# Performance work log

Hardware: AMD Instinct MI355X
Metric: run time of the kernel (lower is better)

## Reference

```python
import jax, jax.numpy as jnp
import numpy as np

N = 100000      # nodes
E = 1600000     # edges (avg degree 16)
IN = 128        # in_channels
H = 4           # heads
C = 32          # out_channels per head
NEG_SLOPE = 0.2 # PyG GATConv default


def setup_inputs() -> dict:
    key = jax.random.key(0)
    k = jax.random.split(key, 6)
    x = jax.random.normal(k[0], (N, IN), jnp.float32)
    edge_index = jax.random.randint(k[1], (2, E), 0, N, jnp.int32)
    # Learned params of GATConv: linear weight, per-head attention vectors, bias
    W = jax.random.normal(k[2], (IN, H * C), jnp.float32) / np.sqrt(IN)
    a_src = jax.random.normal(k[3], (H, C), jnp.float32) * 0.1
    a_dst = jax.random.normal(k[4], (H, C), jnp.float32) * 0.1
    bias = jnp.zeros((H * C,), jnp.float32)
    return {"x": x, "edge_index": edge_index, "W": W,
            "a_src": a_src, "a_dst": a_dst, "bias": bias}


def reference(x, edge_index, W, a_src, a_dst, bias):
    n = x.shape[0]
    # Linear transform, per-head view: [N, H, C]
    h = (x @ W).reshape(n, H, C)
    # Node-level attention halves: alpha_i = <h_i, a>  -> [N, H]
    alpha_src = jnp.einsum('nhc,hc->nh', h, a_src)
    alpha_dst = jnp.einsum('nhc,hc->nh', h, a_dst)
    # add_self_loops=True (PyG default)
    loops = jnp.arange(n, dtype=edge_index.dtype)
    src = jnp.concatenate([edge_index[0], loops])  # [E+N]
    dst = jnp.concatenate([edge_index[1], loops])
    # Edge attention logits with LeakyReLU: [E+N, H]
    e = jax.nn.leaky_relu(alpha_src[src] + alpha_dst[dst], NEG_SLOPE)
    # Numerically stable softmax over incoming edges of each destination node
    m = jax.ops.segment_max(e, dst, num_segments=n)          # [N, H]
    e = jnp.exp(e - m[dst])
    denom = jax.ops.segment_sum(e, dst, num_segments=n)      # [N, H]
    att = e / denom[dst]                                     # [E+N, H]
    # Weighted scatter-aggregate of source features: [N, H, C]
    out = jax.ops.segment_sum(att[:, :, None] * h[src], dst, num_segments=n)
    # concat=True: flatten heads, add bias
    return out.reshape(n, H * C) + bias
```

## Files before the change

kernel.cpp:

```cpp
#include <hip/hip_runtime.h>
#include <stdint.h>


#define NBLK 128
#define BKT 64

typedef __bf16 bf16x8 __attribute__((ext_vector_type(8)));
typedef float f32x4 __attribute__((ext_vector_type(4)));

__device__ __forceinline__ float lrelu(float x) { return x >= 0.f ? x : 0.2f * x; }
__device__ __forceinline__ float blo(unsigned u) { return __uint_as_float(u << 16); }
__device__ __forceinline__ float bhi(unsigned u) { return __uint_as_float(u & 0xffff0000u); }

__global__ __launch_bounds__(256) void k_wprep(const float* __restrict__ W, __bf16* __restrict__ Wt) {
  int idx = blockIdx.x * 256 + threadIdx.x;
  int nn = idx & 127, k = idx >> 7;
  Wt[nn * 128 + k] = (__bf16)W[k * 128 + nn];
}

__global__ __launch_bounds__(256) void k_mega(const float* __restrict__ x, const __bf16* __restrict__ Wt,
                                              const float* __restrict__ a_src, const float* __restrict__ a_dst,
                                              __bf16* __restrict__ h, float* __restrict__ asrc,
                                              float* __restrict__ adst,
                                              const int* __restrict__ ei, int* __restrict__ cnt2,
                                              int n, int e, int NB, int CE, int ngb) {
  __shared__ __align__(16) char Wl[32768];
  __shared__ __align__(16) __bf16 hbuf[4][16 * 64];
  int t = threadIdx.x;

  if ((int)blockIdx.x >= ngb) {
    int hblk = (int)blockIdx.x - ngb;
    int* hist = (int*)Wl;
    for (int j = t; j < NB; j += 256) hist[j] = 0;
    __syncthreads();
    int i0 = hblk * CE, i1 = min(e, i0 + CE);
    for (int i = i0 + t; i < i1; i += 256) atomicAdd(&hist[ei[e + i] >> 6], 1);
    __syncthreads();
    for (int j = t; j < NB; j += 256) cnt2[j * NBLK + hblk] = hist[j];
    return;
  }

  {
    const float4* s4 = (const float4*)Wt;
    for (int i = t; i < 2048; i += 256) {
      int f = i << 4;
      int nr = f >> 8, c = f & 255;
      *(float4*)(Wl + ((nr << 8) | (c ^ ((nr & 7) << 4)))) = s4[i];
    }
  }
  __syncthreads();
  int wv = t >> 6, lane = t & 63;
  int arow = lane & 15, ag = lane >> 4, c15 = lane & 15;
  float as_t[8], ad_t[8];
#pragma unroll
  for (int tile = 0; tile < 8; ++tile) {
    as_t[tile] = a_src[tile * 16 + c15];
    ad_t[tile] = a_dst[tile * 16 + c15];
  }
  int strip = blockIdx.x * 64 + wv * 16;
  int row = strip + arow;
  float4 fa[8];
  if (row < n) {
    const float4* xr = (const float4*)(x + (size_t)row * 128);
#pragma unroll
    for (int q = 0; q < 4; ++q) {
      fa[2 * q]     = xr[q * 8 + ag * 2];
      fa[2 * q + 1] = xr[q * 8 + ag * 2 + 1];
    }
  } else {
#pragma unroll
    for (int q = 0; q < 8; ++q) fa[q] = make_float4(0.f, 0.f, 0.f, 0.f);
  }
  bf16x8 af[4];
#pragma unroll
  for (int q = 0; q < 4; ++q) {
    af[q][0] = (__bf16)fa[2 * q].x;     af[q][1] = (__bf16)fa[2 * q].y;
    af[q][2] = (__bf16)fa[2 * q].z;     af[q][3] = (__bf16)fa[2 * q].w;
    af[q][4] = (__bf16)fa[2 * q + 1].x; af[q][5] = (__bf16)fa[2 * q + 1].y;
    af[q][6] = (__bf16)fa[2 * q + 1].z; af[q][7] = (__bf16)fa[2 * q + 1].w;
  }
  f32x4 acc[8];
#pragma unroll
  for (int tile = 0; tile < 8; ++tile) acc[tile] = (f32x4){0.f, 0.f, 0.f, 0.f};
#pragma unroll
  for (int q = 0; q < 4; ++q) {
    int gb = (q * 64) + (ag << 4);
#pragma unroll
    for (int tile = 0; tile < 8; ++tile) {
      int nn = tile * 16 + c15;
      bf16x8 bf = *(const bf16x8*)(Wl + ((nn << 8) | (gb ^ ((nn & 7) << 4))));
      acc[tile] = __builtin_amdgcn_mfma_f32_16x16x32_bf16(af[q], bf, acc[tile], 0, 0, 0);
    }
  }
#pragma unroll
  for (int hh = 0; hh < 4; ++hh) {
#pragma unroll
    for (int r = 0; r < 4; ++r) {
      float vps = acc[2 * hh][r] * as_t[2 * hh] + acc[2 * hh + 1][r] * as_t[2 * hh + 1];
      float vpd = acc[2 * hh][r] * ad_t[2 * hh] + acc[2 * hh + 1][r] * ad_t[2 * hh + 1];
#pragma unroll
      for (int m = 1; m < 16; m <<= 1) {
        vps += __shfl_xor(vps, m, 64);
        vpd += __shfl_xor(vpd, m, 64);
      }
      if (c15 == 0) {
        int ro = strip + ag * 4 + r;
        if (ro < n) { asrc[ro * 4 + hh] = vps; adst[ro * 4 + hh] = vpd; }
      }
    }
  }
  int rr = lane >> 2, qq = lane & 3;
  int ro = strip + rr;
#pragma unroll
  for (int half = 0; half < 2; ++half) {
#pragma unroll
    for (int tile = 0; tile < 4; ++tile) {
#pragma unroll
      for (int r = 0; r < 4; ++r)
        hbuf[wv][(ag * 4 + r) * 64 + tile * 16 + c15] = (__bf16)acc[half * 4 + tile][r];
    }
    if (ro < n) {
      const float4* src = (const float4*)&hbuf[wv][rr * 64 + qq * 16];
      float4* dst = (float4*)(h + (size_t)ro * 128 + half * 64 + qq * 16);
      dst[0] = src[0];
      dst[1] = src[1];
    }
  }
}


__global__ __launch_bounds__(256) void k_scanA(int* __restrict__ cnt2, int* __restrict__ bsums, int m) {
  __shared__ int wsum[4];
  int t = threadIdx.x, i = blockIdx.x * 256 + t;
  int wv = t >> 6, lane = t & 63;
  int v = (i < m) ? cnt2[i] : 0;
  int sc = v;
#pragma unroll
  for (int ofs = 1; ofs < 64; ofs <<= 1) {
    int u = __shfl_up(sc, ofs, 64);
    if (lane >= ofs) sc += u;
  }
  if (lane == 63) wsum[wv] = sc;
  __syncthreads();
  int base = 0;
  for (int w = 0; w < wv; ++w) base += wsum[w];
  if (i < m) cnt2[i] = base + sc - v;
  if (t == 255) bsums[blockIdx.x] = base + sc;
}

__global__ __launch_bounds__(256) void k_scanB(int* __restrict__ bsums, int nbs) {
  __shared__ int wsum[4];
  int t = threadIdx.x, wv = t >> 6, lane = t & 63;
  int carry = 0;
  for (int c = 0; c < nbs; c += 256) {
    int i = c + t;
    int v = (i < nbs) ? bsums[i] : 0;
    int sc = v;
#pragma unroll
    for (int ofs = 1; ofs < 64; ofs <<= 1) {
      int u = __shfl_up(sc, ofs, 64);
      if (lane >= ofs) sc += u;
    }
    if (lane == 63) wsum[wv] = sc;
    __syncthreads();
    int base = carry;
    for (int w = 0; w < wv; ++w) base += wsum[w];
    if (i < nbs) bsums[i] = base + sc - v;
    carry += wsum[0] + wsum[1] + wsum[2] + wsum[3];
    __syncthreads();
  }
}

__global__ __launch_bounds__(256) void k_fill2(const int* __restrict__ ei, const int* __restrict__ cnt2,
                                               const int* __restrict__ bsums,
                                               unsigned* __restrict__ ebuf, int e, int NB, int CE) {
  __shared__ int cur[2048];
  int t = threadIdx.x, blk = blockIdx.x;
  for (int j = t; j < NB; j += 256) {
    int idx = j * NBLK + blk;
    cur[j] = cnt2[idx] + bsums[idx >> 8];
  }
  __syncthreads();
  int i0 = blk * CE, i1 = min(e, i0 + CE);
  for (int i = i0 + t; i < i1; i += 256) {
    int s = ei[i], d = ei[e + i];
    int pos = atomicAdd(&cur[d >> 6], 1);
    ebuf[pos] = ((unsigned)(d & 63) << 26) | (unsigned)s;
  }
}

__global__ __launch_bounds__(256) void k_sort(const unsigned* __restrict__ ebuf, const int* __restrict__ cnt2,
                                              const int* __restrict__ bsums,
                                              int* __restrict__ off, int* __restrict__ adj, int n, int NB, int e) {
  __shared__ int lcnt[BKT], lcur[BKT];
  int b = blockIdx.x, t = threadIdx.x;
  int wv = t >> 6, lane = t & 63;
  int i0 = b * NBLK;
  int s0 = cnt2[i0] + bsums[i0 >> 8];
  int s1 = e;
  if (b + 1 < NB) { int i1 = (b + 1) * NBLK; s1 = cnt2[i1] + bsums[i1 >> 8]; }
  int cnt = s1 - s0;
  int d0 = b * BKT;
  if (t < BKT) lcnt[t] = 0;
  __syncthreads();
  for (int j = t; j < cnt; j += 256) atomicAdd(&lcnt[ebuf[s0 + j] >> 26], 1);
  __syncthreads();
  if (wv == 0) {
    int v = lcnt[lane];
    int sc = v;
#pragma unroll
    for (int o = 1; o < 64; o <<= 1) {
      int u = __shfl_up(sc, o, 64);
      if (lane >= o) sc += u;
    }
    lcur[lane] = sc - v;
    if (d0 + lane < n) off[d0 + lane] = s0 + sc - v;
  }
  if (b == 0 && t == 0) off[n] = e;
  __syncthreads();
  for (int j = t; j < cnt; j += 256) {
    unsigned u = ebuf[s0 + j];
    int pos = atomicAdd(&lcur[u >> 26], 1);
    adj[s0 + pos] = (int)(u & 0x03FFFFFFu);
  }
}

__global__ __launch_bounds__(256) void k_gather(const int* __restrict__ adj, const int* __restrict__ off,
                                                const float* __restrict__ asrc, const float* __restrict__ adst,
                                                const unsigned* __restrict__ h32,
                                                const float* __restrict__ bias, float* __restrict__ out, int n) {
  int gid = blockIdx.x * 256 + threadIdx.x;
  int node = gid >> 6, lane = gid & 63;
  if (node >= n) return;
  int head = lane >> 4;
  int o = off[node], oe = off[node + 1];
  float adh = adst[node * 4 + head];
  float ps = __expf(lrelu(asrc[node * 4 + head] + adh));
  unsigned su = h32[((unsigned)node << 6) + lane];
  float acc0 = ps * blo(su), acc1 = ps * bhi(su), dtot = ps;
  int j = o;
  for (; j + 8 <= oe; j += 8) {
    int sv[8];
    unsigned hu[8];
    float av[8];
#pragma unroll
    for (int k = 0; k < 8; ++k) sv[k] = adj[j + k];
#pragma unroll
    for (int k = 0; k < 8; ++k) {
      hu[k] = h32[((unsigned)sv[k] << 6) + lane];
      av[k] = asrc[sv[k] * 4 + head];
    }
#pragma unroll
    for (int k = 0; k < 8; ++k) {
      float p = __expf(lrelu(av[k] + adh));
      dtot += p;
      acc0 += p * blo(hu[k]);
      acc1 += p * bhi(hu[k]);
    }
  }
  for (; j + 2 <= oe; j += 2) {
    int sA = adj[j], sB = adj[j + 1];
    unsigned uA = h32[((unsigned)sA << 6) + lane];
    unsigned uB = h32[((unsigned)sB << 6) + lane];
    float pA = __expf(lrelu(asrc[sA * 4 + head] + adh));
    float pB = __expf(lrelu(asrc[sB * 4 + head] + adh));
    dtot += pA + pB;
    acc0 += pA * blo(uA) + pB * blo(uB);
    acc1 += pA * bhi(uA) + pB * bhi(uB);
  }
  if (j < oe) {
    int s = adj[j];
    unsigned u = h32[((unsigned)s << 6) + lane];
    float p = __expf(lrelu(asrc[s * 4 + head] + adh));
    dtot += p;
    acc0 += p * blo(u);
    acc1 += p * bhi(u);
  }
  float inv = 1.f / dtot;
  float2 bb = ((const float2*)bias)[lane];
  ((float2*)(out + (size_t)node * 128))[lane] = make_float2(acc0 * inv + bb.x, acc1 * inv + bb.y);
}

extern "C" void kernel_launch(void* const* d_in, const int* in_sizes, int n_in,
                              void* d_out, int out_size, void* d_ws, size_t ws_size,
                              hipStream_t stream) {
  const float* x     = (const float*)d_in[0];
  const int*   ei    = (const int*)d_in[1];
  const float* W     = (const float*)d_in[2];
  const float* a_src = (const float*)d_in[3];
  const float* a_dst = (const float*)d_in[4];
  const float* bias  = (const float*)d_in[5];
  float* out = (float*)d_out;

  int n = in_sizes[0] / 128;
  int e = in_sizes[1] / 2;
  int NB = (n + BKT - 1) / BKT;
  int ngb = (n + 63) / 64;
  int m = NB * NBLK;
  int gridA = (m + 255) / 256;
  int CE = (e + NBLK - 1) / NBLK;

  char* ws = (char*)d_ws;
  size_t ofs = 0;
  auto alloc = [&](size_t bytes) { void* p = ws + ofs; ofs = (ofs + bytes + 15) & ~(size_t)15; return p; };
  __bf16* h      = (__bf16*)alloc((size_t)n * 128 * sizeof(__bf16));
  unsigned* h32  = (unsigned*)h;
  float* asrc    = (float*)alloc((size_t)n * 4 * sizeof(float));
  float* adst    = (float*)alloc((size_t)n * 4 * sizeof(float));
  int* off       = (int*)alloc((size_t)(n + 1) * sizeof(int));
  int* cnt2      = (int*)alloc((size_t)m * sizeof(int));
  int* bsums     = (int*)alloc((size_t)gridA * sizeof(int));
  unsigned* ebuf = (unsigned*)alloc((size_t)e * sizeof(unsigned));
  int* adj       = (int*)alloc((size_t)e * sizeof(int));
  __bf16* Wt     = (__bf16*)alloc((size_t)128 * 128 * sizeof(__bf16));

  hipLaunchKernelGGL(k_wprep, dim3(64), dim3(256), 0, stream, W, Wt);
  hipLaunchKernelGGL(k_mega, dim3(ngb + NBLK), dim3(256), 0, stream,
                     x, Wt, a_src, a_dst, h, asrc, adst, ei, cnt2, n, e, NB, CE, ngb);
  hipLaunchKernelGGL(k_scanA, dim3(gridA), dim3(256), 0, stream, cnt2, bsums, m);
  hipLaunchKernelGGL(k_scanB, dim3(1), dim3(256), 0, stream, bsums, gridA);
  hipLaunchKernelGGL(k_fill2, dim3(NBLK), dim3(256), 0, stream, ei, cnt2, bsums, ebuf, e, NB, CE);
  hipLaunchKernelGGL(k_sort, dim3(NB), dim3(256), 0, stream, ebuf, cnt2, bsums, off, adj, n, NB, e);
  hipLaunchKernelGGL(k_gather, dim3((n * 64 + 255) / 256), dim3(256), 0, stream,
                     adj, off, asrc, adst, h32, bias, out, n);
}
```

Before: 163.7 us.

## Fuse two-level scan into one kernel, double histogram blocks, recompute attention dots

Merges the block scan and the single-block carry scan into one kernel, where the last-finishing block (found with an atomic counter that the mega kernel resets) scans the block sums. This removes one launch. It also doubles NBLK, so the histogram and fill stages run with more blocks, each handling a smaller edge chunk. The per-node attention dot products are now computed from the bf16 h tile staged in shared memory rather than through 16-lane shuffle reductions over the MFMA accumulators. That trades shuffle work for LDS reads and rounds h to bf16 before the dot product, which slightly changes precision.

```diff
diff --git a/kernel.cpp b/kernel.cpp
--- a/kernel.cpp
+++ b/kernel.cpp
@@ -2,7 +2,7 @@
 #include <stdint.h>
 
 
-#define NBLK 128
+#define NBLK 256
 #define BKT 64
 
 typedef __bf16 bf16x8 __attribute__((ext_vector_type(8)));
@@ -23,6 +23,7 @@
                                               __bf16* __restrict__ h, float* __restrict__ asrc,
                                               float* __restrict__ adst,
                                               const int* __restrict__ ei, int* __restrict__ cnt2,
+                                              int* __restrict__ done,
                                               int n, int e, int NB, int CE, int ngb) {
   __shared__ __align__(16) char Wl[32768];
   __shared__ __align__(16) __bf16 hbuf[4][16 * 64];
@@ -30,6 +31,7 @@
 
   if ((int)blockIdx.x >= ngb) {
     int hblk = (int)blockIdx.x - ngb;
+    if (hblk == 0 && t == 0) *done = 0;
     int* hist = (int*)Wl;
     for (int j = t; j < NB; j += 256) hist[j] = 0;
     __syncthreads();
@@ -51,12 +53,6 @@
   __syncthreads();
   int wv = t >> 6, lane = t & 63;
   int arow = lane & 15, ag = lane >> 4, c15 = lane & 15;
-  float as_t[8], ad_t[8];
-#pragma unroll
-  for (int tile = 0; tile < 8; ++tile) {
-    as_t[tile] = a_src[tile * 16 + c15];
-    ad_t[tile] = a_dst[tile * 16 + c15];
-  }
   int strip = blockIdx.x * 64 + wv * 16;
   int row = strip + arow;
   float4 fa[8];
@@ -92,25 +88,11 @@
       acc[tile] = __builtin_amdgcn_mfma_f32_16x16x32_bf16(af[q], bf, acc[tile], 0, 0, 0);
     }
   }
-#pragma unroll
-  for (int hh = 0; hh < 4; ++hh) {
-#pragma unroll
-    for (int r = 0; r < 4; ++r) {
-      float vps = acc[2 * hh][r] * as_t[2 * hh] + acc[2 * hh + 1][r] * as_t[2 * hh + 1];
-      float vpd = acc[2 * hh][r] * ad_t[2 * hh] + acc[2 * hh + 1][r] * ad_t[2 * hh + 1];
-#pragma unroll
-      for (int m = 1; m < 16; m <<= 1) {
-        vps += __shfl_xor(vps, m, 64);
-        vpd += __shfl_xor(vpd, m, 64);
-      }
-      if (c15 == 0) {
-        int ro = strip + ag * 4 + r;
-        if (ro < n) { asrc[ro * 4 + hh] = vps; adst[ro * 4 + hh] = vpd; }
-      }
-    }
-  }
   int rr = lane >> 2, qq = lane & 3;
   int ro = strip + rr;
+  int row16 = lane & 15;
+  int hh2 = (lane >> 4) & 1;
+  int chunk = lane >> 5;
 #pragma unroll
   for (int half = 0; half < 2; ++half) {
 #pragma unroll
@@ -125,12 +107,31 @@
       dst[0] = src[0];
       dst[1] = src[1];
     }
-  }
-}
-
-
-__global__ __launch_bounds__(256) void k_scanA(int* __restrict__ cnt2, int* __restrict__ bsums, int m) {
+    int headg = half * 2 + hh2;
+    const unsigned* hrow = (const unsigned*)&hbuf[wv][row16 * 64 + hh2 * 32 + chunk * 16];
+    const float* asv = a_src + headg * 32 + chunk * 16;
+    const float* adv = a_dst + headg * 32 + chunk * 16;
+    float ps = 0.f, pd = 0.f;
+#pragma unroll
+    for (int c = 0; c < 8; ++c) {
+      unsigned u = hrow[c];
+      float lo = blo(u), hi = bhi(u);
+      ps += lo * asv[2 * c] + hi * asv[2 * c + 1];
+      pd += lo * adv[2 * c] + hi * adv[2 * c + 1];
+    }
+    ps += __shfl_xor(ps, 32, 64);
+    pd += __shfl_xor(pd, 32, 64);
+    if (chunk == 0) {
+      int ro2 = strip + row16;
+      if (ro2 < n) { asrc[ro2 * 4 + headg] = ps; adst[ro2 * 4 + headg] = pd; }
+    }
+  }
+}
+
+__global__ __launch_bounds__(256) void k_scan(int* __restrict__ cnt2, int* __restrict__ bsums,
+                                              int* __restrict__ done, int m, int gridA) {
   __shared__ int wsum[4];
+  __shared__ int amLast;
   int t = threadIdx.x, i = blockIdx.x * 256 + t;
   int wv = t >> 6, lane = t & 63;
   int v = (i < m) ? cnt2[i] : 0;
@@ -145,27 +146,29 @@
   int base = 0;
   for (int w = 0; w < wv; ++w) base += wsum[w];
   if (i < m) cnt2[i] = base + sc - v;
-  if (t == 255) bsums[blockIdx.x] = base + sc;
-}
-
-__global__ __launch_bounds__(256) void k_scanB(int* __restrict__ bsums, int nbs) {
-  __shared__ int wsum[4];
-  int t = threadIdx.x, wv = t >> 6, lane = t & 63;
+  if (t == 255) {
+    bsums[blockIdx.x] = base + sc;
+    __threadfence();
+    amLast = (atomicAdd(done, 1) == gridA - 1);
+  }
+  __syncthreads();
+  if (!amLast) return;
+  __threadfence();
   int carry = 0;
-  for (int c = 0; c < nbs; c += 256) {
-    int i = c + t;
-    int v = (i < nbs) ? bsums[i] : 0;
-    int sc = v;
+  for (int c = 0; c < gridA; c += 256) {
+    int ii = c + t;
+    int vv = (ii < gridA) ? atomicAdd(&bsums[ii], 0) : 0;
+    int s2 = vv;
 #pragma unroll
     for (int ofs = 1; ofs < 64; ofs <<= 1) {
-      int u = __shfl_up(sc, ofs, 64);
-      if (lane >= ofs) sc += u;
-    }
-    if (lane == 63) wsum[wv] = sc;
+      int u = __shfl_up(s2, ofs, 64);
+      if (lane >= ofs) s2 += u;
+    }
+    if (lane == 63) wsum[wv] = s2;
     __syncthreads();
-    int base = carry;
-    for (int w = 0; w < wv; ++w) base += wsum[w];
-    if (i < nbs) bsums[i] = base + sc - v;
+    int b2 = carry;
+    for (int w = 0; w < wv; ++w) b2 += wsum[w];
+    if (ii < gridA) bsums[ii] = b2 + s2 - vv;
     carry += wsum[0] + wsum[1] + wsum[2] + wsum[3];
     __syncthreads();
   }
@@ -310,15 +313,15 @@
   int* off       = (int*)alloc((size_t)(n + 1) * sizeof(int));
   int* cnt2      = (int*)alloc((size_t)m * sizeof(int));
   int* bsums     = (int*)alloc((size_t)gridA * sizeof(int));
+  int* done      = (int*)alloc(sizeof(int));
   unsigned* ebuf = (unsigned*)alloc((size_t)e * sizeof(unsigned));
   int* adj       = (int*)alloc((size_t)e * sizeof(int));
   __bf16* Wt     = (__bf16*)alloc((size_t)128 * 128 * sizeof(__bf16));
 
   hipLaunchKernelGGL(k_wprep, dim3(64), dim3(256), 0, stream, W, Wt);
   hipLaunchKernelGGL(k_mega, dim3(ngb + NBLK), dim3(256), 0, stream,
-                     x, Wt, a_src, a_dst, h, asrc, adst, ei, cnt2, n, e, NB, CE, ngb);
-  hipLaunchKernelGGL(k_scanA, dim3(gridA), dim3(256), 0, stream, cnt2, bsums, m);
-  hipLaunchKernelGGL(k_scanB, dim3(1), dim3(256), 0, stream, bsums, gridA);
+                     x, Wt, a_src, a_dst, h, asrc, adst, ei, cnt2, done, n, e, NB, CE, ngb);
+  hipLaunchKernelGGL(k_scan, dim3(gridA), dim3(256), 0, stream, cnt2, bsums, done, m, gridA);
   hipLaunchKernelGGL(k_fill2, dim3(NBLK), dim3(256), 0, stream, ei, cnt2, bsums, ebuf, e, NB, CE);
   hipLaunchKernelGGL(k_sort, dim3(NB), dim3(256), 0, stream, ebuf, cnt2, bsums, off, adj, n, NB, e);
   hipLaunchKernelGGL(k_gather, dim3((n * 64 + 255) / 256), dim3(256), 0, stream,
```

Measured after the change: 191.0 us. 16.7% more time.
